# Kernel tuning notes

Measured on AMD Instinct MI355X. Metric: run time of the kernel, lower is better.

Reference implementation:

```python
import jax, jax.numpy as jnp
import numpy as np

N = 100000   # nodes
G = 128      # graphs for mean pool


def gcn_conv(x, edge_index, W, b, num_nodes):
    # PyG GCNConv (default): x' = D^-1/2 (A+I) D^-1/2 (x W) + b
    x = x @ W
    src, dst = edge_index[0], edge_index[1]
    loop = jnp.arange(num_nodes)
    src = jnp.concatenate([src, loop])
    dst = jnp.concatenate([dst, loop])
    ones = jnp.ones(src.shape[0], x.dtype)
    deg = jax.ops.segment_sum(ones, dst, num_segments=num_nodes)
    dinv = jnp.where(deg > 0, jax.lax.rsqrt(deg), 0.0)
    norm = dinv[src] * dinv[dst]            # [E+N]
    msg = x[src] * norm[:, None]            # gather + scale
    out = jax.ops.segment_sum(msg, dst, num_segments=num_nodes)  # scatter-add
    return out + b


def setup_inputs() -> dict:
    key = jax.random.key(0)
    ks = jax.random.split(key, 5)
    x = jax.random.normal(ks[0], (N, 128), jnp.float32)
    edge_index = jax.random.randint(ks[1], (2, 1600000), 0, N)
    batch = jnp.sort(jax.random.randint(ks[2], (N,), 0, G))
    W1 = jax.random.normal(ks[3], (128, 64), jnp.float32) / np.sqrt(128.0)
    b1 = jnp.zeros((64,), jnp.float32)
    W2 = jax.random.normal(ks[4], (64, 64), jnp.float32) / np.sqrt(64.0)
    b2 = jnp.zeros((64,), jnp.float32)
    return {"x": x, "edge_index": edge_index, "batch": batch,
            "W1": W1, "b1": b1, "W2": W2, "b2": b2}


def reference(x, edge_index, batch, W1, b1, W2, b2):
    h = gcn_conv(x, edge_index, W1, b1, N)
    h = jax.nn.relu(h)  # dropout is identity in eval mode
    h = gcn_conv(h, edge_index, W2, b2, N)
    # global_mean_pool over graph ids
    s = jax.ops.segment_sum(h, batch, num_segments=G)
    cnt = jax.ops.segment_sum(jnp.ones((N,), h.dtype), batch, num_segments=G)
    return s / jnp.maximum(cnt, 1.0)[:, None]   # [G, hidden2]
```

## Files before the change

kernel.cpp:

```cpp
#include <hip/hip_runtime.h>
#include <hip/hip_fp16.h>

#define SLOTS 64
#define DEGSTRIDE 16

typedef _Float16 half8 __attribute__((ext_vector_type(8)));
typedef float f32x4 __attribute__((ext_vector_type(4)));

__global__ __launch_bounds__(256) void fused_fill_gemm(
    const int* __restrict__ src, const int* __restrict__ dst, int E, int N,
    int* __restrict__ degp, int* __restrict__ colpad, int chunks,
    const float* __restrict__ in, const float* __restrict__ W,
    __half* __restrict__ out, int tiles) {
  constexpr int K = 128;
  constexpr int LDK = K + 8;
  __shared__ __align__(16) _Float16 Wt[64][LDK];
  int bid = blockIdx.x;

  if (bid < 8 * chunks) {
    int range = bid & 7;
    int chunk = bid >> 3;
    int per = (N + 7) >> 3;
    int lo = range * per, hi = min(N, lo + per);
    int e0 = (int)((long long)chunk * E / chunks);
    int e1 = (int)((long long)(chunk + 1) * E / chunks);
    for (int e = e0 + (int)threadIdx.x; e < e1; e += 256) {
      int d = dst[e];
      if (d >= lo && d < hi) {
        int p = atomicAdd(&degp[(size_t)d * DEGSTRIDE], 1);
        if (p < SLOTS) colpad[(size_t)p * N + d] = src[e];
      }
    }
    return;
  }

  int tile = bid - 8 * chunks;
  if (tile >= tiles) return;
  int t = threadIdx.x;
  int wave = t >> 6, lane = t & 63;
  int arow = lane & 15, kgrp = lane >> 4;
  constexpr int KK = K / 32;
  int row0 = tile * 64;
  int row = row0 + wave * 16 + arow;

  half8 af[KK];
  if (row < N) {
#pragma unroll
    for (int kk = 0; kk < KK; ++kk) {
      const float4* p = (const float4*)&in[(size_t)row * K + kk * 32 + kgrp * 8];
      float4 v0 = p[0], v1 = p[1];
      half8 h;
      h[0] = (_Float16)v0.x; h[1] = (_Float16)v0.y;
      h[2] = (_Float16)v0.z; h[3] = (_Float16)v0.w;
      h[4] = (_Float16)v1.x; h[5] = (_Float16)v1.y;
      h[6] = (_Float16)v1.z; h[7] = (_Float16)v1.w;
      af[kk] = h;
    }
  } else {
#pragma unroll
    for (int kk = 0; kk < KK; ++kk) af[kk] = (half8)((_Float16)0.f);
  }

  for (int j = t; j < K * 64; j += 256) {
    int k = j >> 6, c = j & 63;
    Wt[c][k] = (_Float16)W[j];
  }
  __syncthreads();

  f32x4 acc[4];
#pragma unroll
  for (int ct = 0; ct < 4; ++ct) acc[ct] = (f32x4)(0.f);
#pragma unroll
  for (int kk = 0; kk < KK; ++kk) {
#pragma unroll
    for (int ct = 0; ct < 4; ++ct) {
      half8 b = *(const half8*)&Wt[ct * 16 + arow][kk * 32 + kgrp * 8];
      acc[ct] = __builtin_amdgcn_mfma_f32_16x16x32_f16(af[kk], b, acc[ct], 0, 0, 0);
    }
  }

  int rbase = row0 + wave * 16 + kgrp * 4;
#pragma unroll
  for (int r = 0; r < 4; ++r) {
    int rr = rbase + r;
    if (rr < N) {
#pragma unroll
      for (int ct = 0; ct < 4; ++ct)
        out[(size_t)rr * 64 + ct * 16 + arow] = __float2half(acc[ct][r]);
    }
  }
}

__global__ __launch_bounds__(256) void scale_dinv(const int* __restrict__ degp,
                                                  __half* __restrict__ g,
                                                  float* __restrict__ dinv,
                                                  int* __restrict__ degc, int N) {
  int idx = blockIdx.x * 256 + threadIdx.x;
  if (idx >= N * 8) return;
  int row = idx >> 3;
  int d = degp[(size_t)row * DEGSTRIDE];
  float s = rsqrtf((float)(d + 1));
  half8 h = *(half8*)&g[(size_t)idx * 8];
#pragma unroll
  for (int j = 0; j < 8; ++j) h[j] = (_Float16)((float)h[j] * s);
  *(half8*)&g[(size_t)idx * 8] = h;
  if ((idx & 7) == 0) {
    dinv[row] = s;
    degc[row] = min(d, SLOTS);
  }
}

__global__ __launch_bounds__(256) void aggregate(const __half* __restrict__ g,
                                                 const int* __restrict__ degc,
                                                 const int* __restrict__ colpad,
                                                 const float* __restrict__ dinv,
                                                 const float* __restrict__ bias,
                                                 const int* __restrict__ batch,
                                                 __half* __restrict__ out,
                                                 float* __restrict__ poolsum,
                                                 float* __restrict__ poolcnt,
                                                 int N, int mode) {
  int lane = threadIdx.x & 63;
  int wave = blockIdx.x * 4 + (threadIdx.x >> 6);
  int nwaves = gridDim.x * 4;
  int per = (N + nwaves - 1) / nwaves;
  int n0 = wave * per, n1 = min(N, n0 + per);
  if (n0 >= n1) return;
  float b = (mode == 0) ? bias[lane] : 0.f;
  int cur = mode ? batch[n0] : 0;
  float pacc = 0.f, pcnt = 0.f;
  const int* myplane = colpad + (size_t)lane * N;
  for (int node = n0; node < n1; ++node) {
    int deg = degc[node];
    int nb = (lane < deg) ? myplane[node] : 0;
    float a0 = __half2float(g[(size_t)node * 64 + lane]);
    float a1 = 0.f, a2 = 0.f, a3 = 0.f;
    float a4 = 0.f, a5 = 0.f, a6 = 0.f, a7 = 0.f;
    int j = 0;
    for (; j + 7 < deg; j += 8) {
      int s0 = __shfl(nb, j, 64);
      int s1 = __shfl(nb, j + 1, 64);
      int s2 = __shfl(nb, j + 2, 64);
      int s3 = __shfl(nb, j + 3, 64);
      int s4 = __shfl(nb, j + 4, 64);
      int s5 = __shfl(nb, j + 5, 64);
      int s6 = __shfl(nb, j + 6, 64);
      int s7 = __shfl(nb, j + 7, 64);
      a0 += __half2float(g[(size_t)s0 * 64 + lane]);
      a1 += __half2float(g[(size_t)s1 * 64 + lane]);
      a2 += __half2float(g[(size_t)s2 * 64 + lane]);
      a3 += __half2float(g[(size_t)s3 * 64 + lane]);
      a4 += __half2float(g[(size_t)s4 * 64 + lane]);
      a5 += __half2float(g[(size_t)s5 * 64 + lane]);
      a6 += __half2float(g[(size_t)s6 * 64 + lane]);
      a7 += __half2float(g[(size_t)s7 * 64 + lane]);
    }
    for (; j + 3 < deg; j += 4) {
      int s0 = __shfl(nb, j, 64);
      int s1 = __shfl(nb, j + 1, 64);
      int s2 = __shfl(nb, j + 2, 64);
      int s3 = __shfl(nb, j + 3, 64);
      a0 += __half2float(g[(size_t)s0 * 64 + lane]);
      a1 += __half2float(g[(size_t)s1 * 64 + lane]);
      a2 += __half2float(g[(size_t)s2 * 64 + lane]);
      a3 += __half2float(g[(size_t)s3 * 64 + lane]);
    }
    for (; j < deg; ++j) a0 += __half2float(g[(size_t)__shfl(nb, j, 64) * 64 + lane]);
    float dnode = dinv[node];
    float r = dnode * (((a0 + a1) + (a2 + a3)) + ((a4 + a5) + (a6 + a7))) + b;
    if (mode == 0) {
      out[(size_t)node * 64 + lane] = __float2half(dnode * fmaxf(r, 0.f));
    } else {
      int bg = batch[node];
      if (bg != cur) {
        atomicAdd(&poolsum[cur * 64 + lane], pacc);
        if (lane == 0) atomicAdd(&poolcnt[cur], pcnt);
        pacc = 0.f; pcnt = 0.f; cur = bg;
      }
      pacc += r; pcnt += 1.f;
    }
  }
  if (mode) {
    atomicAdd(&poolsum[cur * 64 + lane], pacc);
    if (lane == 0) atomicAdd(&poolcnt[cur], pcnt);
  }
}

__global__ __launch_bounds__(64) void finalize_gemm(const float* __restrict__ poolsum,
                                                    const float* __restrict__ poolcnt,
                                                    const float* __restrict__ W2,
                                                    const float* __restrict__ b2,
                                                    float* __restrict__ out, int Gn) {
  __shared__ float m[64];
  int g = blockIdx.x, c = threadIdx.x;
  float cnt = poolcnt[g];
  float inv = (cnt > 0.f) ? 1.f / cnt : 0.f;
  m[c] = poolsum[g * 64 + c] * inv;
  __syncthreads();
  float acc = 0.f;
#pragma unroll
  for (int k = 0; k < 64; ++k) acc = fmaf(m[k], W2[k * 64 + c], acc);
  out[g * 64 + c] = (cnt > 0.f) ? acc + b2[c] : 0.f;
}

extern "C" void kernel_launch(void* const* d_in, const int* in_sizes, int n_in,
                              void* d_out, int out_size, void* d_ws, size_t ws_size,
                              hipStream_t stream) {
  const float* x   = (const float*)d_in[0];
  const int* ei    = (const int*)d_in[1];
  const int* batch = (const int*)d_in[2];
  const float* W1  = (const float*)d_in[3];
  const float* b1  = (const float*)d_in[4];
  const float* W2  = (const float*)d_in[5];
  const float* b2  = (const float*)d_in[6];
  float* out = (float*)d_out;

  int N  = in_sizes[2];
  int E  = in_sizes[1] / 2;
  int Gn = out_size / 64;

  char* ws = (char*)d_ws;
  size_t off = 0;
  auto alloc = [&](size_t bytes) -> void* {
    void* p = ws + off;
    off = (off + bytes + 255) & ~(size_t)255;
    return p;
  };
  float* poolsum = (float*)alloc(4ull * Gn * 64);
  float* poolcnt = (float*)alloc(4ull * Gn);
  size_t zero_bytes = off;
  int* colpad    = (int*)alloc(4ull * (size_t)N * SLOTS);
  float* dinv    = (float*)alloc(4ull * N);
  int* degc      = (int*)alloc(4ull * N);
  __half* gbuf   = (__half*)alloc(2ull * (size_t)N * 64);
  __half* ybuf   = (__half*)alloc(2ull * (size_t)N * 64);
  int* degp = (int*)ybuf;
  (void)ws_size; (void)n_in;

  hipMemsetAsync(poolsum, 0, zero_bytes, stream);
  hipMemsetAsync(degp, 0, 4ull * (size_t)N * DEGSTRIDE, stream);

  const int* srcv = ei;
  const int* dstv = ei + E;
  int tiles64 = (N + 63) / 64;
  int chunks = 256;

  fused_fill_gemm<<<8 * chunks + tiles64, 256, 0, stream>>>(
      srcv, dstv, E, N, degp, colpad, chunks, x, W1, gbuf, tiles64);
  scale_dinv<<<(N * 8 + 255) / 256, 256, 0, stream>>>(degp, gbuf, dinv, degc, N);

  aggregate<<<2048, 256, 0, stream>>>(gbuf, degc, colpad, dinv, b1, batch, ybuf,
                                      nullptr, nullptr, N, 0);
  aggregate<<<2048, 256, 0, stream>>>(ybuf, degc, colpad, dinv, b1, batch, nullptr,
                                      poolsum, poolcnt, N, 1);
  finalize_gemm<<<Gn, 64, 0, stream>>>(poolsum, poolcnt, W2, b2, out, Gn);
}
```

Measured before the change: 298.7 us.

## Split edge fill from GEMM and fold degree scaling into GEMM epilogue

Separates the edge-fill phase into its own kernel that processes each edge once, with no 8-way destination-range filtering. The first-layer GEMM now runs after the fill and applies the D^-1/2 row scaling and the dinv/degc writes in its epilogue, which removes the separate scale_dinv pass over the feature buffer. The trade-off is that the GEMM can no longer overlap with the fill. The fill also loses the destination-range partitioning that kept its atomics and scattered writes localized.

```diff
diff --git a/kernel.cpp b/kernel.cpp
--- a/kernel.cpp
+++ b/kernel.cpp
@@ -7,40 +7,34 @@
 typedef _Float16 half8 __attribute__((ext_vector_type(8)));
 typedef float f32x4 __attribute__((ext_vector_type(4)));
 
-__global__ __launch_bounds__(256) void fused_fill_gemm(
-    const int* __restrict__ src, const int* __restrict__ dst, int E, int N,
-    int* __restrict__ degp, int* __restrict__ colpad, int chunks,
-    const float* __restrict__ in, const float* __restrict__ W,
-    __half* __restrict__ out, int tiles) {
+__global__ __launch_bounds__(256) void fill_pad(const int* __restrict__ src,
+                                                const int* __restrict__ dst, int E, int N,
+                                                int* __restrict__ degp,
+                                                int* __restrict__ colpad, int chunks) {
+  int chunk = blockIdx.x;
+  int e0 = (int)((long long)chunk * E / chunks);
+  int e1 = (int)((long long)(chunk + 1) * E / chunks);
+  for (int e = e0 + (int)threadIdx.x; e < e1; e += 256) {
+    int d = dst[e];
+    int p = atomicAdd(&degp[(size_t)d * DEGSTRIDE], 1);
+    if (p < SLOTS) colpad[(size_t)p * N + d] = src[e];
+  }
+}
+
+__global__ __launch_bounds__(256) void gemm_scale(const float* __restrict__ in,
+                                                  const float* __restrict__ W,
+                                                  const int* __restrict__ degp,
+                                                  float* __restrict__ dinv,
+                                                  int* __restrict__ degc,
+                                                  __half* __restrict__ out, int N) {
   constexpr int K = 128;
   constexpr int LDK = K + 8;
   __shared__ __align__(16) _Float16 Wt[64][LDK];
-  int bid = blockIdx.x;
-
-  if (bid < 8 * chunks) {
-    int range = bid & 7;
-    int chunk = bid >> 3;
-    int per = (N + 7) >> 3;
-    int lo = range * per, hi = min(N, lo + per);
-    int e0 = (int)((long long)chunk * E / chunks);
-    int e1 = (int)((long long)(chunk + 1) * E / chunks);
-    for (int e = e0 + (int)threadIdx.x; e < e1; e += 256) {
-      int d = dst[e];
-      if (d >= lo && d < hi) {
-        int p = atomicAdd(&degp[(size_t)d * DEGSTRIDE], 1);
-        if (p < SLOTS) colpad[(size_t)p * N + d] = src[e];
-      }
-    }
-    return;
-  }
-
-  int tile = bid - 8 * chunks;
-  if (tile >= tiles) return;
   int t = threadIdx.x;
   int wave = t >> 6, lane = t & 63;
   int arow = lane & 15, kgrp = lane >> 4;
   constexpr int KK = K / 32;
-  int row0 = tile * 64;
+  int row0 = blockIdx.x * 64;
   int row = row0 + wave * 16 + arow;
 
   half8 af[KK];
@@ -60,6 +54,18 @@
 #pragma unroll
     for (int kk = 0; kk < KK; ++kk) af[kk] = (half8)((_Float16)0.f);
   }
+  int rbase = row0 + wave * 16 + kgrp * 4;
+  float dv[4];
+#pragma unroll
+  for (int r = 0; r < 4; ++r)
+    dv[r] = (rbase + r < N)
+        ? rsqrtf((float)(degp[(size_t)(rbase + r) * DEGSTRIDE] + 1))
+        : 0.f;
+  if (t < 64 && row0 + t < N) {
+    int d = degp[(size_t)(row0 + t) * DEGSTRIDE];
+    dinv[row0 + t] = rsqrtf((float)(d + 1));
+    degc[row0 + t] = min(d, SLOTS);
+  }
 
   for (int j = t; j < K * 64; j += 256) {
     int k = j >> 6, c = j & 63;
@@ -79,34 +85,14 @@
     }
   }
 
-  int rbase = row0 + wave * 16 + kgrp * 4;
 #pragma unroll
   for (int r = 0; r < 4; ++r) {
     int rr = rbase + r;
     if (rr < N) {
 #pragma unroll
       for (int ct = 0; ct < 4; ++ct)
-        out[(size_t)rr * 64 + ct * 16 + arow] = __float2half(acc[ct][r]);
-    }
-  }
-}
-
-__global__ __launch_bounds__(256) void scale_dinv(const int* __restrict__ degp,
-                                                  __half* __restrict__ g,
-                                                  float* __restrict__ dinv,
-                                                  int* __restrict__ degc, int N) {
-  int idx = blockIdx.x * 256 + threadIdx.x;
-  if (idx >= N * 8) return;
-  int row = idx >> 3;
-  int d = degp[(size_t)row * DEGSTRIDE];
-  float s = rsqrtf((float)(d + 1));
-  half8 h = *(half8*)&g[(size_t)idx * 8];
-#pragma unroll
-  for (int j = 0; j < 8; ++j) h[j] = (_Float16)((float)h[j] * s);
-  *(half8*)&g[(size_t)idx * 8] = h;
-  if ((idx & 7) == 0) {
-    dinv[row] = s;
-    degc[row] = min(d, SLOTS);
+        out[(size_t)rr * 64 + ct * 16 + arow] = __float2half(acc[ct][r] * dv[r]);
+    }
   }
 }
 
@@ -243,11 +229,9 @@
   const int* srcv = ei;
   const int* dstv = ei + E;
   int tiles64 = (N + 63) / 64;
-  int chunks = 256;
-
-  fused_fill_gemm<<<8 * chunks + tiles64, 256, 0, stream>>>(
-      srcv, dstv, E, N, degp, colpad, chunks, x, W1, gbuf, tiles64);
-  scale_dinv<<<(N * 8 + 255) / 256, 256, 0, stream>>>(degp, gbuf, dinv, degc, N);
+
+  fill_pad<<<2048, 256, 0, stream>>>(srcv, dstv, E, N, degp, colpad, 2048);
+  gemm_scale<<<tiles64, 256, 0, stream>>>(x, W1, degp, dinv, degc, gbuf, N);
 
   aggregate<<<2048, 256, 0, stream>>>(gbuf, degc, colpad, dinv, b1, batch, ybuf,
                                       nullptr, nullptr, N, 0);
```

Result: slower. 342.6 us (+14.7%).
